# Kernel optimization log

Hardware: AMD Instinct MI355X
Metric: run time of the kernel (lower is better)

## Reference

```python
import jax, jax.numpy as jnp
import numpy as np

N, C = 65536, 100
TEMP = 2.0


def setup_inputs() -> dict:
    key = jax.random.key(0)
    ks = jax.random.split(key, 7)
    inp = {}
    names = ["outputs1", "outputs2", "outputs3", "outputs4", "outputs5", "mimic"]
    for k, name in zip(ks[:6], names):
        inp[name] = jax.random.normal(k, (N, C), dtype=jnp.float32)
    inp["targets"] = jax.random.randint(ks[6], (N,), 0, C, dtype=jnp.int64)
    inp["n_test"] = N
    return inp


def _margin(x, targets):
    # top-2 values per row; margin = top1-top2 if the target class is the argmax, else 0
    top2, _ = jax.lax.top_k(x, 2)  # [N, 2]
    tgt_val = jnp.take_along_axis(x, targets[:, None], axis=1)[:, 0]  # [N]
    return jnp.where(tgt_val == top2[:, 0], top2[:, 0] - top2[:, 1],
                     jnp.zeros((), dtype=x.dtype))


def reference(outputs1, outputs2, outputs3, outputs4, outputs5, mimic, targets, n_test):
    margins = jnp.stack(
        [_margin(o, targets) for o in (outputs1, outputs2, outputs3, outputs4, outputs5, mimic)],
        axis=-1,
    )  # [n_test, 6]
    out_threshold = jax.nn.softmax(margins / TEMP, axis=-1)
    max_preds = jnp.max(jnp.stack([outputs1, outputs2, outputs3, outputs4, outputs5], axis=0))
    return (max_preds, out_threshold)
```

## Files before the change

### kernel.cpp

```cpp
#include <hip/hip_runtime.h>


constexpr int C       = 100;
constexpr int ROWS    = 64;
constexpr float INV_TEMP = 0.5f;

__device__ __forceinline__ unsigned enc_f(float f) {
    unsigned u = __float_as_uint(f);
    return (u & 0x80000000u) ? ~u : (u | 0x80000000u);
}

__device__ __forceinline__ void async_cp16(const float* g, float* l) {
    __builtin_amdgcn_global_load_lds(
        (const __attribute__((address_space(1))) void*)g,
        (__attribute__((address_space(3))) void*)l,
        16, 0, 0);
}

__global__ __launch_bounds__(256) void margin_kernel(
    const float* __restrict__ o1, const float* __restrict__ o2,
    const float* __restrict__ o3, const float* __restrict__ o4,
    const float* __restrict__ o5, const float* __restrict__ mimic,
    const int* __restrict__ tgt, float* __restrict__ out,
    unsigned* __restrict__ ws, int n)
{
    __shared__ float    tile[ROWS * C];
    __shared__ unsigned wmax[4];

    const int m    = blockIdx.y;
    const int tid  = threadIdx.x;
    const int lane = tid & 63;

    const float* __restrict__ mat =
        (m == 0) ? o1 : (m == 1) ? o2 : (m == 2) ? o3 :
        (m == 3) ? o4 : (m == 4) ? o5 : mimic;

    const int pidx  = 2 * lane + 1;
    const int probe = (pidx < n) ? tgt[pidx] : 0;
    const unsigned long long nz = __ballot(probe != 0);
    const int tstride = (nz == 0ull) ? 2 : 1;

    const size_t base   = (size_t)blockIdx.x * (ROWS * C);
    const size_t maxIdx = (size_t)n * C - 4;
    #pragma unroll
    for (int c = 0; c < 6; ++c) {
        const int    off = (c * 256 + tid) * 4;
        const size_t g   = base + (size_t)off;
        async_cp16(mat + (g <= maxIdx ? g : maxIdx), tile + off);
    }
    if (tid < 64) {
        const int    off = 6 * 1024 + tid * 4;
        const size_t g   = base + (size_t)off;
        async_cp16(mat + (g <= maxIdx ? g : maxIdx), tile + off);
    }
    __syncthreads();

    const int rl  = tid >> 2;
    const int q   = tid & 3;
    const int row = blockIdx.x * ROWS + rl;

    const float* p = tile + rl * C + q * 25;
    float a1 = -INFINITY, a2 = -INFINITY;
    float b1 = -INFINITY, b2 = -INFINITY;
    #pragma unroll
    for (int i = 0; i < 12; ++i) {
        const float va = p[2 * i], vb = p[2 * i + 1];
        a2 = fmaxf(a2, fminf(a1, va)); a1 = fmaxf(a1, va);
        b2 = fmaxf(b2, fminf(b1, vb)); b1 = fmaxf(b1, vb);
    }
    { const float v = p[24]; a2 = fmaxf(a2, fminf(a1, v)); a1 = fmaxf(a1, v); }
    float m1 = fmaxf(a1, b1);
    float m2 = fmaxf(fminf(a1, b1), fmaxf(a2, b2));

    #pragma unroll
    for (int s = 1; s <= 2; s <<= 1) {
        const float p1 = __shfl_xor(m1, s);
        const float p2 = __shfl_xor(m2, s);
        m2 = fmaxf(fminf(m1, p1), fmaxf(m2, p2));
        m1 = fmaxf(m1, p1);
    }

    if (q == 0 && row < n) {
        const int   t  = tgt[(size_t)row * tstride];
        const float tv = tile[rl * C + t];
        out[1 + (size_t)row * 6 + m] = (tv == m1) ? (m1 - m2) * INV_TEMP : 0.0f;
    }

    float gm = (row < n) ? m1 : -INFINITY;
    #pragma unroll
    for (int s = 1; s < 64; s <<= 1) gm = fmaxf(gm, __shfl_xor(gm, s));
    if (m < 5) {
        if (lane == 0) wmax[tid >> 6] = enc_f(gm);
        __syncthreads();
        if (tid == 0)
            atomicMax(ws, max(max(wmax[0], wmax[1]), max(wmax[2], wmax[3])));
    }
}

__global__ __launch_bounds__(256) void softmax_kernel(
    float* __restrict__ out, const unsigned* __restrict__ ws, int n)
{
    const int row = blockIdx.x * blockDim.x + threadIdx.x;
    if (row < n) {
        float* p = out + 1 + (size_t)row * 6;
        float mrg[6];
        #pragma unroll
        for (int j = 0; j < 6; ++j) mrg[j] = p[j];
        float mx = mrg[0];
        #pragma unroll
        for (int j = 1; j < 6; ++j) mx = fmaxf(mx, mrg[j]);
        float e[6], s = 0.0f;
        #pragma unroll
        for (int j = 0; j < 6; ++j) { e[j] = __expf(mrg[j] - mx); s += e[j]; }
        const float inv = 1.0f / s;
        #pragma unroll
        for (int j = 0; j < 6; ++j) p[j] = e[j] * inv;
    }
    if (row == 0) {
        const unsigned e = ws[0];
        const unsigned bits = (e & 0x80000000u) ? (e & 0x7FFFFFFFu) : ~e;
        out[0] = __uint_as_float(bits);
    }
}

extern "C" void kernel_launch(void* const* d_in, const int* in_sizes, int n_in,
                              void* d_out, int out_size, void* d_ws, size_t ws_size,
                              hipStream_t stream) {
    const float* o1    = (const float*)d_in[0];
    const float* o2    = (const float*)d_in[1];
    const float* o3    = (const float*)d_in[2];
    const float* o4    = (const float*)d_in[3];
    const float* o5    = (const float*)d_in[4];
    const float* mimic = (const float*)d_in[5];
    const int*   tgt   = (const int*)d_in[6];
    float*       out   = (float*)d_out;
    unsigned*    ws    = (unsigned*)d_ws;

    const int n = in_sizes[6];

    hipMemsetAsync(ws, 0, sizeof(unsigned), stream);

    dim3 grid((n + ROWS - 1) / ROWS, 6);
    margin_kernel<<<grid, 256, 0, stream>>>(o1, o2, o3, o4, o5, mimic,
                                            tgt, out, ws, n);
    softmax_kernel<<<(n + 255) / 256, 256, 0, stream>>>(out, ws, n);
}
```

Baseline: 205.8 us.

## Load rows directly into registers as float4 instead of staging through LDS

```diff
diff --git a/kernel.cpp b/kernel.cpp
--- a/kernel.cpp
+++ b/kernel.cpp
@@ -1,8 +1,7 @@
 #include <hip/hip_runtime.h>
 
 
-constexpr int C       = 100;
-constexpr int ROWS    = 64;
+constexpr int C = 100;
 constexpr float INV_TEMP = 0.5f;
 
 __device__ __forceinline__ unsigned enc_f(float f) {
@@ -10,11 +9,36 @@
     return (u & 0x80000000u) ? ~u : (u | 0x80000000u);
 }
 
-__device__ __forceinline__ void async_cp16(const float* g, float* l) {
-    __builtin_amdgcn_global_load_lds(
-        (const __attribute__((address_space(1))) void*)g,
-        (__attribute__((address_space(3))) void*)l,
-        16, 0, 0);
+__device__ __forceinline__ void t2(float& m1, float& m2, float v) {
+    m2 = fmaxf(m2, fminf(m1, v));
+    m1 = fmaxf(m1, v);
+}
+
+__device__ __forceinline__ void row_top2(const float4 v0, const float4 v1,
+                                         const float4 v2, const float4 v3,
+                                         float& M1, float& M2) {
+    float a1=-INFINITY,a2=-INFINITY,b1=-INFINITY,b2=-INFINITY;
+    float c1=-INFINITY,c2=-INFINITY,d1=-INFINITY,d2=-INFINITY;
+    t2(a1,a2,v0.x); t2(b1,b2,v0.y); t2(c1,c2,v0.z); t2(d1,d2,v0.w);
+    t2(a1,a2,v1.x); t2(b1,b2,v1.y); t2(c1,c2,v1.z); t2(d1,d2,v1.w);
+    t2(a1,a2,v2.x); t2(b1,b2,v2.y); t2(c1,c2,v2.z); t2(d1,d2,v2.w);
+    t2(a1,a2,v3.x); t2(b1,b2,v3.y); t2(c1,c2,v3.z); t2(d1,d2,v3.w);
+    const float ab1 = fmaxf(a1,b1), ab2 = fmaxf(fminf(a1,b1), fmaxf(a2,b2));
+    const float cd1 = fmaxf(c1,d1), cd2 = fmaxf(fminf(c1,d1), fmaxf(c2,d2));
+    M1 = fmaxf(ab1, cd1);
+    M2 = fmaxf(fminf(ab1, cd1), fmaxf(ab2, cd2));
+}
+
+__device__ __forceinline__ float tgt_cand(int t, int sub,
+                                          const float4 v0, const float4 v1,
+                                          const float4 v2, const float4 v3) {
+    const int fidx  = t >> 2;
+    const int comp  = t & 3;
+    const int owner = (fidx < 24) ? (fidx & 7) : 0;
+    if (sub != owner) return -INFINITY;
+    const int regi  = (fidx < 24) ? (fidx >> 3) : 3;
+    const float4 v  = (regi == 0) ? v0 : (regi == 1) ? v1 : (regi == 2) ? v2 : v3;
+    return (comp == 0) ? v.x : (comp == 1) ? v.y : (comp == 2) ? v.z : v.w;
 }
 
 __global__ __launch_bounds__(256) void margin_kernel(
@@ -24,12 +48,14 @@
     const int* __restrict__ tgt, float* __restrict__ out,
     unsigned* __restrict__ ws, int n)
 {
-    __shared__ float    tile[ROWS * C];
     __shared__ unsigned wmax[4];
 
     const int m    = blockIdx.y;
     const int tid  = threadIdx.x;
     const int lane = tid & 63;
+    const int sub  = lane & 7;
+    const int rg   = lane >> 3;
+    const int wv   = tid >> 6;
 
     const float* __restrict__ mat =
         (m == 0) ? o1 : (m == 1) ? o2 : (m == 2) ? o3 :
@@ -40,57 +66,61 @@
     const unsigned long long nz = __ballot(probe != 0);
     const int tstride = (nz == 0ull) ? 2 : 1;
 
-    const size_t base   = (size_t)blockIdx.x * (ROWS * C);
-    const size_t maxIdx = (size_t)n * C - 4;
-    #pragma unroll
-    for (int c = 0; c < 6; ++c) {
-        const int    off = (c * 256 + tid) * 4;
-        const size_t g   = base + (size_t)off;
-        async_cp16(mat + (g <= maxIdx ? g : maxIdx), tile + off);
+    const int rowA0 = blockIdx.x * 64 + wv * 16 + rg;
+    const int rowB0 = rowA0 + 8;
+    const int rowA  = min(rowA0, n - 1);
+    const int rowB  = min(rowB0, n - 1);
+
+    const float4* __restrict__ pA = (const float4*)(mat + (size_t)rowA * C);
+    const float4* __restrict__ pB = (const float4*)(mat + (size_t)rowB * C);
+
+    const float4 vA0 = pA[sub], vA1 = pA[8 + sub], vA2 = pA[16 + sub];
+    const float4 vB0 = pB[sub], vB1 = pB[8 + sub], vB2 = pB[16 + sub];
+    float4 vA3 = make_float4(-INFINITY, -INFINITY, -INFINITY, -INFINITY);
+    float4 vB3 = vA3;
+    int tA = 0, tB = 0;
+    if (sub == 0) {
+        vA3 = pA[24];
+        vB3 = pB[24];
+        tA  = tgt[(size_t)rowA * tstride];
+        tB  = tgt[(size_t)rowB * tstride];
     }
-    if (tid < 64) {
-        const int    off = 6 * 1024 + tid * 4;
-        const size_t g   = base + (size_t)off;
-        async_cp16(mat + (g <= maxIdx ? g : maxIdx), tile + off);
-    }
-    __syncthreads();
+    tA = __shfl(tA, lane & 56);
+    tB = __shfl(tB, lane & 56);
 
-    const int rl  = tid >> 2;
-    const int q   = tid & 3;
-    const int row = blockIdx.x * ROWS + rl;
-
-    const float* p = tile + rl * C + q * 25;
-    float a1 = -INFINITY, a2 = -INFINITY;
-    float b1 = -INFINITY, b2 = -INFINITY;
-    #pragma unroll
-    for (int i = 0; i < 12; ++i) {
-        const float va = p[2 * i], vb = p[2 * i + 1];
-        a2 = fmaxf(a2, fminf(a1, va)); a1 = fmaxf(a1, va);
-        b2 = fmaxf(b2, fminf(b1, vb)); b1 = fmaxf(b1, vb);
-    }
-    { const float v = p[24]; a2 = fmaxf(a2, fminf(a1, v)); a1 = fmaxf(a1, v); }
-    float m1 = fmaxf(a1, b1);
-    float m2 = fmaxf(fminf(a1, b1), fmaxf(a2, b2));
+    float m1A, m2A, m1B, m2B;
+    row_top2(vA0, vA1, vA2, vA3, m1A, m2A);
+    row_top2(vB0, vB1, vB2, vB3, m1B, m2B);
+    float cA = tgt_cand(tA, sub, vA0, vA1, vA2, vA3);
+    float cB = tgt_cand(tB, sub, vB0, vB1, vB2, vB3);
 
     #pragma unroll
-    for (int s = 1; s <= 2; s <<= 1) {
-        const float p1 = __shfl_xor(m1, s);
-        const float p2 = __shfl_xor(m2, s);
-        m2 = fmaxf(fminf(m1, p1), fmaxf(m2, p2));
-        m1 = fmaxf(m1, p1);
+    for (int s = 1; s <= 4; s <<= 1) {
+        const float o1A = __shfl_xor(m1A, s), o2A = __shfl_xor(m2A, s);
+        const float ocA = __shfl_xor(cA, s);
+        m2A = fmaxf(fminf(m1A, o1A), fmaxf(m2A, o2A));
+        m1A = fmaxf(m1A, o1A);
+        cA  = fmaxf(cA, ocA);
+        const float o1B = __shfl_xor(m1B, s), o2B = __shfl_xor(m2B, s);
+        const float ocB = __shfl_xor(cB, s);
+        m2B = fmaxf(fminf(m1B, o1B), fmaxf(m2B, o2B));
+        m1B = fmaxf(m1B, o1B);
+        cB  = fmaxf(cB, ocB);
     }
 
-    if (q == 0 && row < n) {
-        const int   t  = tgt[(size_t)row * tstride];
-        const float tv = tile[rl * C + t];
-        out[1 + (size_t)row * 6 + m] = (tv == m1) ? (m1 - m2) * INV_TEMP : 0.0f;
+    if (sub == 0) {
+        if (rowA0 < n)
+            out[1 + (size_t)rowA0 * 6 + m] = (cA == m1A) ? (m1A - m2A) * INV_TEMP : 0.0f;
+        if (rowB0 < n)
+            out[1 + (size_t)rowB0 * 6 + m] = (cB == m1B) ? (m1B - m2B) * INV_TEMP : 0.0f;
     }
 
-    float gm = (row < n) ? m1 : -INFINITY;
+    float gm = fmaxf(rowA0 < n ? m1A : -INFINITY,
+                     rowB0 < n ? m1B : -INFINITY);
     #pragma unroll
     for (int s = 1; s < 64; s <<= 1) gm = fmaxf(gm, __shfl_xor(gm, s));
     if (m < 5) {
-        if (lane == 0) wmax[tid >> 6] = enc_f(gm);
+        if (lane == 0) wmax[wv] = enc_f(gm);
         __syncthreads();
         if (tid == 0)
             atomicMax(ws, max(max(wmax[0], wmax[1]), max(wmax[2], wmax[3])));
@@ -140,7 +170,7 @@
 
     hipMemsetAsync(ws, 0, sizeof(unsigned), stream);
 
-    dim3 grid((n + ROWS - 1) / ROWS, 6);
+    dim3 grid((n + 63) / 64, 6);
     margin_kernel<<<grid, 256, 0, stream>>>(o1, o2, o3, o4, o5, mimic,
                                             tgt, out, ws, n);
     softmax_kernel<<<(n + 255) / 256, 256, 0, stream>>>(out, ws, n);
```

New measurement: 202.3 us. About the same (-1.7%).
